# Performance work log

Hardware: AMD Instinct MI355X
Metric: run time of the kernel (lower is better)

Reference implementation:

```python
import jax, jax.numpy as jnp
import numpy as np

_LUM = jnp.array([0.299, 0.587, 0.114], dtype=jnp.float32)


def setup_inputs() -> dict:
    key = jax.random.key(0)
    k1, k2 = jax.random.split(key)
    B, H, W = 4, 1024, 1024
    grid = jax.random.normal(k1, (B, 12, 16, 16, 8), dtype=jnp.float32)
    image = jax.random.uniform(k2, (B, 3, H, W), dtype=jnp.float32)
    return {"grid": grid, "image": image}


def _trilinear_sample(G, x, y, z):
    """Faithful port of F.grid_sample (5D, bilinear, border, align_corners=True).

    G: (B, C, D, Hg, Wg). Coords in [-1,1]: x -> Wg axis, y -> Hg axis, z -> D axis.
    x, y, z: (B, H, W). Returns (B, H, W, C).
    """
    B, C, D, Hg, Wg = G.shape

    def unnorm(c, size):
        u = (c + 1.0) * 0.5 * (size - 1)  # align_corners=True
        return jnp.clip(u, 0.0, size - 1)  # border padding

    ux, uy, uz = unnorm(x, Wg), unnorm(y, Hg), unnorm(z, D)
    x0 = jnp.floor(ux).astype(jnp.int32)
    y0 = jnp.floor(uy).astype(jnp.int32)
    z0 = jnp.floor(uz).astype(jnp.int32)
    x1 = jnp.minimum(x0 + 1, Wg - 1)
    y1 = jnp.minimum(y0 + 1, Hg - 1)
    z1 = jnp.minimum(z0 + 1, D - 1)
    wx = (ux - x0)[..., None]
    wy = (uy - y0)[..., None]
    wz = (uz - z0)[..., None]

    Gt = jnp.transpose(G, (0, 2, 3, 4, 1))  # (B, D, Hg, Wg, C)
    bb = jnp.arange(B)[:, None, None]

    def g(zi, yi, xi):
        return Gt[bb, zi, yi, xi]  # (B, H, W, C)

    c00 = g(z0, y0, x0) * (1 - wx) + g(z0, y0, x1) * wx
    c01 = g(z0, y1, x0) * (1 - wx) + g(z0, y1, x1) * wx
    c10 = g(z1, y0, x0) * (1 - wx) + g(z1, y0, x1) * wx
    c11 = g(z1, y1, x0) * (1 - wx) + g(z1, y1, x1) * wx
    c0 = c00 * (1 - wy) + c01 * wy
    c1 = c10 * (1 - wy) + c11 * wy
    return c0 * (1 - wz) + c1 * wz


def reference(grid, image):
    B, C, H, W = image.shape
    out_ch, in_ch = 3, 3
    n_mat = out_ch * in_ch

    guide = jnp.einsum('bchw,c->bhw', image, _LUM)  # luminance guide
    gx = jnp.linspace(0.0, 1.0, W) * 2.0 - 1.0  # image x -> grid_sample x (last axis)
    gy = jnp.linspace(0.0, 1.0, H) * 2.0 - 1.0  # image y -> grid_sample y
    xb = jnp.broadcast_to(gx[None, None, :], (B, H, W))
    yb = jnp.broadcast_to(gy[None, :, None], (B, H, W))
    zb = guide * 2.0 - 1.0  # guide -> grid_sample z (depth axis)

    coeffs = _trilinear_sample(grid, xb, yb, zb)  # (B, H, W, 12)
    A = coeffs[..., :n_mat].reshape(B, H, W, out_ch, in_ch)
    bias = coeffs[..., n_mat:]  # (B, H, W, out_ch)

    img_hwc = jnp.transpose(image, (0, 2, 3, 1))  # (B, H, W, in_ch)
    out = jnp.einsum('bhwoi,bhwi->bhwo', A, img_hwc) + bias
    out = jnp.clip(out, 0.0, 1.0)
    return jnp.transpose(out, (0, 3, 1, 2))  # (B, out_ch, H, W)
```

## Files before the change

### kernel.cpp

```cpp
#include <hip/hip_runtime.h>

#define BB 4
#define HH 1024
#define WW 1024
#define NC 12
#define GD 16
#define GH 16
#define GW 8

#define ZSD 12
#define XSD 196
#define HSZ (GW * XSD)

typedef _Float16 h2 __attribute__((ext_vector_type(2)));
union HU { uint u; h2 h; };

#define CH(ua_, ub_, dst_) do {                                   \
    HU A_, B_; A_.u = (ua_); B_.u = (ub_);                        \
    h2 m_ = A_.h + wx2 * (B_.h - A_.h);                           \
    float m0_ = (float)m_.x;                                      \
    float m1_ = (float)m_.y;                                      \
    dst_ = fmaf(wz, m1_ - m0_, m0_);                              \
} while (0)

__global__ __launch_bounds__(256) void bgrid_row(const float* __restrict__ img,
                                                 const float* __restrict__ grid,
                                                 float* __restrict__ out)
{
    const int y = blockIdx.x;
    const int b = blockIdx.y;
    const int tid = threadIdx.x;

    __shared__ __align__(16) uint H[HSZ];

    float uy = fminf(y * (15.0f / 1023.0f), 15.0f);
    int y0 = (int)uy;
    int y1 = min(y0 + 1, GH - 1);
    float wy = uy - (float)y0;

    const float* gb = grid + (size_t)b * (NC * GD * GH * GW);
#pragma unroll
    for (int j = 0; j < 6; j++) {
        int t = tid + 256 * j;
        int x = t & 7;
        int z = (t >> 3) & 15;
        int c = t >> 7;
        int zp = min(z + 1, GD - 1);
        const float* bc = gb + c * (GD * GH * GW) + x;
        float a0 = bc[(z  * GH + y0) * GW];
        float a1 = bc[(z  * GH + y1) * GW];
        float c0 = bc[(zp * GH + y0) * GW];
        float c1 = bc[(zp * GH + y1) * GW];
        float f0 = fmaf(wy, a1 - a0, a0);
        float f1 = fmaf(wy, c1 - c0, c0);
        HU pk;
        pk.h = h2{(_Float16)f0, (_Float16)f1};
        H[x * XSD + z * ZSD + c] = pk.u;
    }
    __syncthreads();

    const size_t plane = (size_t)HH * WW;
    const size_t rowoff = (size_t)b * 3 * plane + (size_t)y * WW;
    const float4 r4 = *(const float4*)(img + rowoff + 4 * tid);
    const float4 g4 = *(const float4*)(img + rowoff + plane + 4 * tid);
    const float4 b4 = *(const float4*)(img + rowoff + 2 * plane + 4 * tid);

    float4 o0, o1, o2;
    float* o0p = (float*)&o0; float* o1p = (float*)&o1; float* o2p = (float*)&o2;
    const float* rp = (const float*)&r4;
    const float* gp = (const float*)&g4;
    const float* bp = (const float*)&b4;

#pragma unroll
    for (int p = 0; p < 4; p++) {
        const int px = 4 * tid + p;
        const float r = rp[p], g = gp[p], bl = bp[p];

        float ux = fminf(px * (7.0f / 1023.0f), 7.0f);
        int x0 = (int)ux;
        int x1 = min(x0 + 1, GW - 1);
        float wx = ux - (float)x0;
        _Float16 wxh = (_Float16)wx;
        h2 wx2 = h2{wxh, wxh};

        float lum = 0.299f * r + 0.587f * g + 0.114f * bl;
        float uz = fminf(fmaxf(lum * 15.0f, 0.0f), 15.0f);
        int z0 = (int)uz;
        float wz = uz - (float)z0;

        const uint* pa = &H[x0 * XSD + z0 * ZSD];
        const uint* pb = &H[x1 * XSD + z0 * ZSD];
        const uint4 qa0 = ((const uint4*)pa)[0];
        const uint4 qa1 = ((const uint4*)pa)[1];
        const uint4 qa2 = ((const uint4*)pa)[2];
        const uint4 qb0 = ((const uint4*)pb)[0];
        const uint4 qb1 = ((const uint4*)pb)[1];
        const uint4 qb2 = ((const uint4*)pb)[2];

        float c0, c1, c2, c3, c4, c5, c6, c7, c8, c9, c10, c11;
        CH(qa0.x, qb0.x, c0);  CH(qa0.y, qb0.y, c1);
        CH(qa0.z, qb0.z, c2);  CH(qa0.w, qb0.w, c3);
        CH(qa1.x, qb1.x, c4);  CH(qa1.y, qb1.y, c5);
        CH(qa1.z, qb1.z, c6);  CH(qa1.w, qb1.w, c7);
        CH(qa2.x, qb2.x, c8);  CH(qa2.y, qb2.y, c9);
        CH(qa2.z, qb2.z, c10); CH(qa2.w, qb2.w, c11);

        float v0 = c0 * r + c1 * g + c2  * bl + c9;
        float v1 = c3 * r + c4 * g + c5  * bl + c10;
        float v2 = c6 * r + c7 * g + c8  * bl + c11;
        o0p[p] = fminf(fmaxf(v0, 0.0f), 1.0f);
        o1p[p] = fminf(fmaxf(v1, 0.0f), 1.0f);
        o2p[p] = fminf(fmaxf(v2, 0.0f), 1.0f);
    }

    *(float4*)(out + rowoff + 4 * tid) = o0;
    *(float4*)(out + rowoff + plane + 4 * tid) = o1;
    *(float4*)(out + rowoff + 2 * plane + 4 * tid) = o2;
}

extern "C" void kernel_launch(void* const* d_in, const int* in_sizes, int n_in,
                              void* d_out, int out_size, void* d_ws, size_t ws_size,
                              hipStream_t stream) {
    const float* grid  = (const float*)d_in[0];
    const float* image = (const float*)d_in[1];
    float* out = (float*)d_out;

    dim3 blk(256);
    dim3 grd(HH, BB);
    bgrid_row<<<grd, blk, 0, stream>>>(image, grid, out);
}
```

Baseline: 24.76 us.

## Process four image rows per block with shared grid slice and nontemporal IO

Each block now handles four consecutive rows, building four y-interpolated grid slices in LDS. When all four rows fall in the same grid cell, it reuses one set of grid loads. Image loads are issued early, before and after the slice build, so they overlap with it, and global loads and stores use nontemporal hints to reduce cache pollution. The trade-off is four times fewer blocks and higher LDS and register use per block, which may lower occupancy.

```diff
diff --git a/kernel.cpp b/kernel.cpp
--- a/kernel.cpp
+++ b/kernel.cpp
@@ -13,6 +13,7 @@
 #define HSZ (GW * XSD)
 
 typedef _Float16 h2 __attribute__((ext_vector_type(2)));
+typedef float f4 __attribute__((ext_vector_type(4)));
 union HU { uint u; h2 h; };
 
 #define CH(ua_, ub_, dst_) do {                                   \
@@ -23,58 +24,21 @@
     dst_ = fmaf(wz, m1_ - m0_, m0_);                              \
 } while (0)
 
-__global__ __launch_bounds__(256) void bgrid_row(const float* __restrict__ img,
-                                                 const float* __restrict__ grid,
-                                                 float* __restrict__ out)
+__device__ __forceinline__ f4 ntld(const float* p) {
+    return __builtin_nontemporal_load((const f4*)p);
+}
+
+__device__ __forceinline__ void run4(const uint* __restrict__ Hs,
+                                     const f4& r4, const f4& g4, const f4& b4,
+                                     float* __restrict__ outp, int tid,
+                                     size_t plane)
 {
-    const int y = blockIdx.x;
-    const int b = blockIdx.y;
-    const int tid = threadIdx.x;
-
-    __shared__ __align__(16) uint H[HSZ];
-
-    float uy = fminf(y * (15.0f / 1023.0f), 15.0f);
-    int y0 = (int)uy;
-    int y1 = min(y0 + 1, GH - 1);
-    float wy = uy - (float)y0;
-
-    const float* gb = grid + (size_t)b * (NC * GD * GH * GW);
-#pragma unroll
-    for (int j = 0; j < 6; j++) {
-        int t = tid + 256 * j;
-        int x = t & 7;
-        int z = (t >> 3) & 15;
-        int c = t >> 7;
-        int zp = min(z + 1, GD - 1);
-        const float* bc = gb + c * (GD * GH * GW) + x;
-        float a0 = bc[(z  * GH + y0) * GW];
-        float a1 = bc[(z  * GH + y1) * GW];
-        float c0 = bc[(zp * GH + y0) * GW];
-        float c1 = bc[(zp * GH + y1) * GW];
-        float f0 = fmaf(wy, a1 - a0, a0);
-        float f1 = fmaf(wy, c1 - c0, c0);
-        HU pk;
-        pk.h = h2{(_Float16)f0, (_Float16)f1};
-        H[x * XSD + z * ZSD + c] = pk.u;
-    }
-    __syncthreads();
-
-    const size_t plane = (size_t)HH * WW;
-    const size_t rowoff = (size_t)b * 3 * plane + (size_t)y * WW;
-    const float4 r4 = *(const float4*)(img + rowoff + 4 * tid);
-    const float4 g4 = *(const float4*)(img + rowoff + plane + 4 * tid);
-    const float4 b4 = *(const float4*)(img + rowoff + 2 * plane + 4 * tid);
-
-    float4 o0, o1, o2;
-    float* o0p = (float*)&o0; float* o1p = (float*)&o1; float* o2p = (float*)&o2;
-    const float* rp = (const float*)&r4;
-    const float* gp = (const float*)&g4;
-    const float* bp = (const float*)&b4;
+    f4 o0, o1, o2;
 
 #pragma unroll
     for (int p = 0; p < 4; p++) {
         const int px = 4 * tid + p;
-        const float r = rp[p], g = gp[p], bl = bp[p];
+        const float r = r4[p], g = g4[p], bl = b4[p];
 
         float ux = fminf(px * (7.0f / 1023.0f), 7.0f);
         int x0 = (int)ux;
@@ -88,8 +52,8 @@
         int z0 = (int)uz;
         float wz = uz - (float)z0;
 
-        const uint* pa = &H[x0 * XSD + z0 * ZSD];
-        const uint* pb = &H[x1 * XSD + z0 * ZSD];
+        const uint* pa = Hs + x0 * XSD + z0 * ZSD;
+        const uint* pb = Hs + x1 * XSD + z0 * ZSD;
         const uint4 qa0 = ((const uint4*)pa)[0];
         const uint4 qa1 = ((const uint4*)pa)[1];
         const uint4 qa2 = ((const uint4*)pa)[2];
@@ -108,14 +72,100 @@
         float v0 = c0 * r + c1 * g + c2  * bl + c9;
         float v1 = c3 * r + c4 * g + c5  * bl + c10;
         float v2 = c6 * r + c7 * g + c8  * bl + c11;
-        o0p[p] = fminf(fmaxf(v0, 0.0f), 1.0f);
-        o1p[p] = fminf(fmaxf(v1, 0.0f), 1.0f);
-        o2p[p] = fminf(fmaxf(v2, 0.0f), 1.0f);
+        o0[p] = fminf(fmaxf(v0, 0.0f), 1.0f);
+        o1[p] = fminf(fmaxf(v1, 0.0f), 1.0f);
+        o2[p] = fminf(fmaxf(v2, 0.0f), 1.0f);
     }
 
-    *(float4*)(out + rowoff + 4 * tid) = o0;
-    *(float4*)(out + rowoff + plane + 4 * tid) = o1;
-    *(float4*)(out + rowoff + 2 * plane + 4 * tid) = o2;
+    __builtin_nontemporal_store(o0, (f4*)(outp + 4 * tid));
+    __builtin_nontemporal_store(o1, (f4*)(outp + 4 * tid + plane));
+    __builtin_nontemporal_store(o2, (f4*)(outp + 4 * tid + 2 * plane));
+}
+
+__global__ __launch_bounds__(256) void bgrid_row4(const float* __restrict__ img,
+                                                  const float* __restrict__ grid,
+                                                  float* __restrict__ out)
+{
+    const int yb = blockIdx.x * 4;
+    const int b = blockIdx.y;
+    const int tid = threadIdx.x;
+
+    __shared__ __align__(16) uint H[4][HSZ];
+
+    const size_t plane = (size_t)HH * WW;
+    const size_t rbase = (size_t)b * 3 * plane + (size_t)yb * WW;
+    const float* ip = img + rbase + 4 * tid;
+
+    const f4 rA = ntld(ip);
+    const f4 gA = ntld(ip + plane);
+    const f4 bA = ntld(ip + 2 * plane);
+    const f4 rB = ntld(ip + WW);
+    const f4 gB = ntld(ip + WW + plane);
+    const f4 bB = ntld(ip + WW + 2 * plane);
+
+    float uyv[4]; int y0v[4]; int y1v[4];
+#pragma unroll
+    for (int r = 0; r < 4; r++) {
+        float uy = fminf((yb + r) * (15.0f / 1023.0f), 15.0f);
+        uyv[r] = uy;
+        y0v[r] = (int)uy;
+        y1v[r] = min(y0v[r] + 1, GH - 1);
+    }
+    const bool same_cell = (y0v[0] == y0v[3]);
+
+    const float* gbase = grid + (size_t)b * (NC * GD * GH * GW);
+#pragma unroll
+    for (int j = 0; j < 6; j++) {
+        int t = tid + 256 * j;
+        int x = t & 7;
+        int z = (t >> 3) & 15;
+        int c = t >> 7;
+        int zp = min(z + 1, GD - 1);
+        const float* bc = gbase + c * (GD * GH * GW) + x;
+        int off = x * XSD + z * ZSD + c;
+        if (same_cell) {
+            const int ya0 = y0v[0], ya1 = y1v[0];
+            float a0 = bc[(z  * GH + ya0) * GW];
+            float a1 = bc[(z  * GH + ya1) * GW];
+            float e0 = bc[(zp * GH + ya0) * GW];
+            float e1 = bc[(zp * GH + ya1) * GW];
+            float d0 = a1 - a0, d1 = e1 - e0;
+#pragma unroll
+            for (int r = 0; r < 4; r++) {
+                float w = uyv[r] - (float)ya0;
+                HU pk;
+                pk.h = h2{(_Float16)fmaf(w, d0, a0), (_Float16)fmaf(w, d1, e0)};
+                H[r][off] = pk.u;
+            }
+        } else {
+#pragma unroll
+            for (int r = 0; r < 4; r++) {
+                const int yy0 = y0v[r], yy1 = y1v[r];
+                float a0 = bc[(z  * GH + yy0) * GW];
+                float a1 = bc[(z  * GH + yy1) * GW];
+                float e0 = bc[(zp * GH + yy0) * GW];
+                float e1 = bc[(zp * GH + yy1) * GW];
+                float w = uyv[r] - (float)yy0;
+                HU pk;
+                pk.h = h2{(_Float16)fmaf(w, a1 - a0, a0), (_Float16)fmaf(w, e1 - e0, e0)};
+                H[r][off] = pk.u;
+            }
+        }
+    }
+
+    const f4 rC = ntld(ip + 2 * WW);
+    const f4 gC = ntld(ip + 2 * WW + plane);
+    const f4 bC = ntld(ip + 2 * WW + 2 * plane);
+    const f4 rD = ntld(ip + 3 * WW);
+    const f4 gD = ntld(ip + 3 * WW + plane);
+    const f4 bD = ntld(ip + 3 * WW + 2 * plane);
+
+    __syncthreads();
+
+    run4(H[0], rA, gA, bA, out + rbase,          tid, plane);
+    run4(H[1], rB, gB, bB, out + rbase + WW,     tid, plane);
+    run4(H[2], rC, gC, bC, out + rbase + 2 * WW, tid, plane);
+    run4(H[3], rD, gD, bD, out + rbase + 3 * WW, tid, plane);
 }
 
 extern "C" void kernel_launch(void* const* d_in, const int* in_sizes, int n_in,
@@ -126,6 +176,6 @@
     float* out = (float*)d_out;
 
     dim3 blk(256);
-    dim3 grd(HH, BB);
-    bgrid_row<<<grd, blk, 0, stream>>>(image, grid, out);
+    dim3 grd(HH / 4, BB);
+    bgrid_row4<<<grd, blk, 0, stream>>>(image, grid, out);
 }
```

New measurement: 28.63 us. +15.6%, slower.
